# Optimization experiments

Hardware: AMD Instinct MI355X
Metric: run time of the kernel (lower is better)

Reference implementation:

```python
import jax, jax.numpy as jnp
import numpy as np

N_NODES = 50000
N_EDGES = 800000
IN, S1, S2, S3 = 64, 128, 64, 32


def _lin_init(key, fan_in, fan_out):
    kw, kb = jax.random.split(key)
    s = 1.0 / np.sqrt(fan_in)
    W = jax.random.uniform(kw, (fan_in, fan_out), minval=-s, maxval=s, dtype=jnp.float32)
    b = jax.random.uniform(kb, (fan_out,), minval=-s, maxval=s, dtype=jnp.float32)
    return W, b


def setup_inputs() -> dict:
    key = jax.random.key(0)
    ks = jax.random.split(key, 11)
    x = jax.random.normal(ks[0], (N_NODES, IN), dtype=jnp.float32)
    src = jax.random.randint(ks[1], (N_EDGES,), 0, N_NODES)
    dst = jax.random.randint(ks[2], (N_EDGES,), 0, N_NODES)
    W_n1, b_n1 = _lin_init(ks[3], IN, S1)
    W_c1, b_c1 = _lin_init(ks[4], S1, S2)
    W_n2, b_n2 = _lin_init(ks[5], S1, S2)
    W_c2, b_c2 = _lin_init(ks[6], S2, S3)
    W_n3, b_n3 = _lin_init(ks[7], S2, S3)
    W_c3, b_c3 = _lin_init(ks[8], S3, 1)
    W_g1, b_g1 = _lin_init(ks[9], S2, S3)
    W_g2, b_g2 = _lin_init(ks[10], S3, 1)
    return {
        'pre_node_embedding': x, 'src': src, 'dst': dst,
        'W_n1': W_n1, 'b_n1': b_n1, 'W_c1': W_c1, 'b_c1': b_c1,
        'W_n2': W_n2, 'b_n2': b_n2, 'W_c2': W_c2, 'b_c2': b_c2,
        'W_n3': W_n3, 'b_n3': b_n3, 'W_c3': W_c3, 'b_c3': b_c3,
        'W_g1': W_g1, 'b_g1': b_g1, 'W_g2': W_g2, 'b_g2': b_g2,
    }


def _node_update(W, b, emb, src, dst, n_nodes):
    # gather neighbor states along edges, scatter-add onto destinations
    agg = jax.ops.segment_sum(emb[src], dst, num_segments=n_nodes)  # [N, d_in]
    return jax.nn.sigmoid((emb + agg) @ W + b)                      # [N, d_out]


def _conduit_update(W, b, emb, src, dst):
    # conduit (edge) embedding from its two endpoint nodes
    return jax.nn.sigmoid((emb[src] + emb[dst]) @ W + b)            # [E, d_out]


def reference(pre_node_embedding, src, dst,
              W_n1, b_n1, W_c1, b_c1, W_n2, b_n2, W_c2, b_c2,
              W_n3, b_n3, W_c3, b_c3, W_g1, b_g1, W_g2, b_g2):
    n = pre_node_embedding.shape[0]
    h1 = _node_update(W_n1, b_n1, pre_node_embedding, src, dst, n)  # [N, S1]
    c1 = _conduit_update(W_c1, b_c1, h1, src, dst)                  # [E, S2]
    h2 = _node_update(W_n2, b_n2, h1, src, dst, n)                  # [N, S2]
    c2 = _conduit_update(W_c2, b_c2, h2, src, dst)                  # [E, S3]
    g1 = jax.nn.sigmoid(c1 @ W_g1 + b_g1 + c2)                      # [E, S3]
    h3 = _node_update(W_n3, b_n3, h2, src, dst, n)                  # [N, S3]
    c3 = _conduit_update(W_c3, b_c3, h3, src, dst)                  # [E, 1]
    out = jax.nn.sigmoid(g1 @ W_g2 + b_g2 + c3)                     # [E, 1]
    return out
```

## Files before the change

### kernel.cpp

```cpp
#include <hip/hip_runtime.h>

#define N_NODES 50000
#define N_EDGES 800000
#define CVT_B 6250
#define NODE_B ((N_NODES + 63) / 64)
#define EDGE_B (N_EDGES / 128)
#define NB 196
#define FILL_B 196
#define FILL_CHUNK 4096

typedef _Float16 h2 __attribute__((ext_vector_type(2)));
typedef _Float16 f16x8 __attribute__((ext_vector_type(8)));
typedef float f32x4 __attribute__((ext_vector_type(4)));

__device__ __forceinline__ float sigf(float v) {
  return __builtin_amdgcn_rcpf(1.0f + __expf(-v));
}
__device__ __forceinline__ unsigned packh2(float a, float b) {
  return __builtin_bit_cast(unsigned, __builtin_amdgcn_cvt_pkrtz(a, b));
}
__device__ __forceinline__ float2 unpackh2(unsigned u) {
  h2 p = __builtin_bit_cast(h2, u);
  return make_float2((float)p.x, (float)p.y);
}
__device__ __forceinline__ void acc8(float* a, uint4 v) {
  float2 p0 = unpackh2(v.x), p1 = unpackh2(v.y);
  float2 p2 = unpackh2(v.z), p3 = unpackh2(v.w);
  a[0] += p0.x; a[1] += p0.y; a[2] += p1.x; a[3] += p1.y;
  a[4] += p2.x; a[5] += p2.y; a[6] += p3.x; a[7] += p3.y;
}
__device__ __forceinline__ unsigned addpk(unsigned a, unsigned b) {
  h2 r = __builtin_bit_cast(h2, a) + __builtin_bit_cast(h2, b);
  return __builtin_bit_cast(unsigned, r);
}
#define MFMA16(A, B, C) __builtin_amdgcn_mfma_f32_16x16x32_f16(A, __builtin_bit_cast(f16x8, B), C, 0, 0, 0)

__global__ __launch_bounds__(256) void prep_kernel(
    const float* __restrict__ x, unsigned* __restrict__ x16,
    const float* __restrict__ Wn1, const float* __restrict__ Wn2,
    const float* __restrict__ Wc1, const float* __restrict__ Wn3,
    const float* __restrict__ Wc2, const float* __restrict__ Wg1,
    uint4* __restrict__ Wn1f, uint4* __restrict__ Wn2f, uint4* __restrict__ Wc1f,
    uint4* __restrict__ Wn3f, uint4* __restrict__ Wc2f, uint4* __restrict__ Wg1f)
{
  int b = blockIdx.x;
  if (b < CVT_B) {
    int i = b * 256 + threadIdx.x;
    float2 v = ((const float2*)x)[i];
    x16[i] = packh2(v.x, v.y);
  } else {
    int lane = threadIdx.x & 63, w = threadIdx.x >> 6;
    int n15 = lane & 15, chunk = lane >> 4;
    if (w == 0) {
#pragma unroll
      for (int f = 0; f < 16; ++f) {
        int nt = f >> 1, ks = f & 1;
        int n = nt * 16 + n15;
        f16x8 vv;
#pragma unroll
        for (int i = 0; i < 8; ++i) vv[i] = (_Float16)Wn1[(ks * 32 + chunk * 8 + i) * 128 + n];
        Wn1f[f * 64 + lane] = __builtin_bit_cast(uint4, vv);
      }
    } else if (w == 1) {
#pragma unroll
      for (int f = 0; f < 16; ++f) {
        int nt = f >> 2, ks = f & 3;
        int n = nt * 16 + n15;
        f16x8 vv;
#pragma unroll
        for (int i = 0; i < 8; ++i) vv[i] = (_Float16)Wn2[(ks * 32 + chunk * 8 + i) * 64 + n];
        Wn2f[f * 64 + lane] = __builtin_bit_cast(uint4, vv);
      }
    } else if (w == 2) {
#pragma unroll
      for (int f = 0; f < 16; ++f) {
        int nt = f >> 2, ks = f & 3;
        int n = nt * 16 + n15;
        f16x8 vv;
#pragma unroll
        for (int i = 0; i < 8; ++i) vv[i] = (_Float16)Wc1[(ks * 32 + chunk * 8 + i) * 64 + n];
        Wc1f[f * 64 + lane] = __builtin_bit_cast(uint4, vv);
      }
    } else {
#pragma unroll
      for (int f = 0; f < 4; ++f) {
        int nt = f >> 1, ks = f & 1;
        int n = nt * 16 + n15;
        f16x8 v3, vc;
#pragma unroll
        for (int i = 0; i < 8; ++i) {
          int k = ks * 32 + chunk * 8 + i;
          v3[i] = (_Float16)Wn3[k * 32 + n];
          vc[i] = (_Float16)Wc2[k * 32 + n];
        }
        Wn3f[f * 64 + lane] = __builtin_bit_cast(uint4, v3);
        Wc2f[f * 64 + lane] = __builtin_bit_cast(uint4, vc);
      }
#pragma unroll
      for (int ks = 0; ks < 2; ++ks)
#pragma unroll
        for (int nh = 0; nh < 2; ++nh) {
          f16x8 vv;
#pragma unroll
          for (int i = 0; i < 8; ++i)
            vv[i] = (_Float16)Wg1[(ks * 32 + chunk * 8 + i) * 32 + nh * 16 + n15];
          Wg1f[(ks * 2 + nh) * 64 + lane] = __builtin_bit_cast(uint4, vv);
        }
    }
  }
}

__global__ __launch_bounds__(256) void fill1_kernel(
    const int* __restrict__ dst, int* __restrict__ histM)
{
  __shared__ int hist[NB];
  int tid = threadIdx.x, bid = blockIdx.x;
  if (tid < NB) hist[tid] = 0;
  __syncthreads();
  int ebase = bid * FILL_CHUNK;
#pragma unroll
  for (int it = 0; it < FILL_CHUNK / 256; ++it) {
    int e = ebase + it * 256 + tid;
    if (e < N_EDGES) atomicAdd(&hist[dst[e] >> 8], 1);
  }
  __syncthreads();
  if (tid < NB) histM[bid * NB + tid] = hist[tid];
}

__global__ __launch_bounds__(256) void scanA_kernel(
    const int* __restrict__ histM, int* __restrict__ colOff,
    int* __restrict__ bucketBase)
{
  int j = threadIdx.x, lane = j & 63, w = j >> 6;
  int total = 0;
  if (j < NB)
    for (int i = 0; i < FILL_B; ++i) total += histM[i * NB + j];
  int x = total;
#pragma unroll
  for (int off = 1; off < 64; off <<= 1) {
    int y = __shfl_up(x, off);
    if (lane >= off) x += y;
  }
  __shared__ int ws[4];
  if (lane == 63) ws[w] = x;
  __syncthreads();
  int woff = 0;
#pragma unroll
  for (int k = 0; k < 4; ++k) if (k < w) woff += ws[k];
  int excl = woff + x - total;
  if (j < NB) {
    bucketBase[j] = excl;
    int running = excl;
    for (int i = 0; i < FILL_B; ++i) {
      colOff[i * NB + j] = running;
      running += histM[i * NB + j];
    }
    if (j == NB - 1) bucketBase[NB] = running;
  }
}

__global__ __launch_bounds__(256) void fill2_kernel(
    const int* __restrict__ src, const int* __restrict__ dst,
    const int* __restrict__ colOff, uint2* __restrict__ cem)
{
  __shared__ int cur[NB];
  int tid = threadIdx.x, bid = blockIdx.x;
  if (tid < NB) cur[tid] = colOff[bid * NB + tid];
  __syncthreads();
  int ebase = bid * FILL_CHUNK;
#pragma unroll
  for (int it = 0; it < FILL_CHUNK / 256; ++it) {
    int e = ebase + it * 256 + tid;
    if (e < N_EDGES) {
      int s = src[e], d = dst[e];
      int pos = atomicAdd(&cur[d >> 8], 1);
      cem[pos] = make_uint2((unsigned)s, ((unsigned)(d & 255) << 20) | (unsigned)e);
    }
  }
}

__global__ __launch_bounds__(256) void fill3_kernel(
    const uint2* __restrict__ cem, const int* __restrict__ bucketBase,
    uint2* __restrict__ ce, int* __restrict__ rowptr, int* __restrict__ did)
{
  __shared__ int cnt[256], curs[256], ws[4];
  int j = blockIdx.x, tid = threadIdx.x;
  int base = bucketBase[j], endb = bucketBase[j + 1];
  cnt[tid] = 0;
  __syncthreads();
  for (int k = base + tid; k < endb; k += 256)
    atomicAdd(&cnt[(cem[k].y >> 20) & 255], 1);
  __syncthreads();
  int v = cnt[tid];
  int lane = tid & 63, w = tid >> 6;
  int x = v;
#pragma unroll
  for (int off = 1; off < 64; off <<= 1) {
    int y = __shfl_up(x, off);
    if (lane >= off) x += y;
  }
  if (lane == 63) ws[w] = x;
  __syncthreads();
  int woff = 0;
#pragma unroll
  for (int k = 0; k < 4; ++k) if (k < w) woff += ws[k];
  int ex = woff + x - v;
  curs[tid] = ex;
  int n = j * 256 + tid;
  if (n < N_NODES) {
    rowptr[n + 1] = base + ex + v;
    if (n == 0) rowptr[0] = 0;
    for (int k2 = 0; k2 < v; ++k2) did[base + ex + k2] = n;
  }
  __syncthreads();
  for (int k = base + tid; k < endb; k += 256) {
    uint2 r = cem[k];
    int dlow = (r.y >> 20) & 255;
    int pos = base + atomicAdd(&curs[dlow], 1);
    ce[pos] = make_uint2(r.x, r.y & 0xFFFFFu);
  }
}

__global__ __launch_bounds__(256) void gather1_kernel(
    const unsigned* __restrict__ X16, const int* __restrict__ rowptr,
    const int* __restrict__ ce2, unsigned* __restrict__ T16)
{
  int w = threadIdx.x >> 6, lane = threadIdx.x & 63;
  int n = blockIdx.x * 4 + w;
  if (n >= N_NODES) return;
  int beg = rowptr[n], end = rowptr[n + 1];
  int q = lane >> 3, c = lane & 7;
  const uint4* feat4 = (const uint4*)X16;
  float a[8] = {0.f, 0.f, 0.f, 0.f, 0.f, 0.f, 0.f, 0.f};
  for (int k0 = beg; k0 < end; k0 += 64) {
    int kk = k0 + lane;
    int cv = (kk < end) ? ce2[2 * kk] : 0;
    int m = end - k0; if (m > 64) m = 64;
    int e = 0;
#pragma unroll 2
    for (; e + 7 < m; e += 8) {
      int se = __shfl(cv, e + q);
      acc8(a, feat4[(size_t)se * 8 + c]);
    }
    int r = m - e;
    if (r) {
      int idx = e + q; if (idx >= m) idx = m - 1;
      int se = __shfl(cv, idx);
      uint4 v = feat4[(size_t)se * 8 + c];
      if (q < r) acc8(a, v);
    }
  }
#pragma unroll
  for (int j = 0; j < 8; ++j) {
    a[j] += __shfl_xor(a[j], 32);
    a[j] += __shfl_xor(a[j], 16);
    a[j] += __shfl_xor(a[j], 8);
  }
  if (q == 0) {
    uint4 xv = ((const uint4*)X16)[(size_t)n * 8 + c];
    float2 x0 = unpackh2(xv.x), x1 = unpackh2(xv.y);
    float2 x2 = unpackh2(xv.z), x3 = unpackh2(xv.w);
    uint4 o;
    o.x = packh2(a[0] + x0.x, a[1] + x0.y);
    o.y = packh2(a[2] + x1.x, a[3] + x1.y);
    o.z = packh2(a[4] + x2.x, a[5] + x2.y);
    o.w = packh2(a[6] + x3.x, a[7] + x3.y);
    ((uint4*)T16)[(size_t)n * 8 + c] = o;
  }
}

__global__ __launch_bounds__(256) void gather2_kernel(
    const unsigned* __restrict__ Q2u, const int* __restrict__ rowptr,
    const int* __restrict__ ce2, const float* __restrict__ bn2,
    unsigned* __restrict__ H2)
{
  int w = threadIdx.x >> 6, lane = threadIdx.x & 63;
  int n = blockIdx.x * 4 + w;
  if (n >= N_NODES) return;
  int beg = rowptr[n], end = rowptr[n + 1];
  int q = lane >> 3, c = lane & 7;
  const uint4* feat4 = (const uint4*)Q2u;
  float a[8] = {0.f, 0.f, 0.f, 0.f, 0.f, 0.f, 0.f, 0.f};
  for (int k0 = beg; k0 < end; k0 += 64) {
    int kk = k0 + lane;
    int cv = (kk < end) ? ce2[2 * kk] : 0;
    int m = end - k0; if (m > 64) m = 64;
    int e = 0;
#pragma unroll 2
    for (; e + 7 < m; e += 8) {
      int se = __shfl(cv, e + q);
      acc8(a, feat4[(size_t)se * 8 + c]);
    }
    int r = m - e;
    if (r) {
      int idx = e + q; if (idx >= m) idx = m - 1;
      int se = __shfl(cv, idx);
      uint4 v = feat4[(size_t)se * 8 + c];
      if (q < r) acc8(a, v);
    }
  }
#pragma unroll
  for (int j = 0; j < 8; ++j) {
    a[j] += __shfl_xor(a[j], 32);
    a[j] += __shfl_xor(a[j], 16);
    a[j] += __shfl_xor(a[j], 8);
  }
  if (q == 0) {
    uint4 qv = ((const uint4*)Q2u)[(size_t)n * 8 + c];
    float4 bnA = ((const float4*)bn2)[2 * c];
    float4 bnB = ((const float4*)bn2)[2 * c + 1];
    float2 q0 = unpackh2(qv.x), q1 = unpackh2(qv.y);
    float2 q2 = unpackh2(qv.z), q3 = unpackh2(qv.w);
    uint4 o;
    o.x = packh2(sigf(a[0] + q0.x + bnA.x), sigf(a[1] + q0.y + bnA.y));
    o.y = packh2(sigf(a[2] + q1.x + bnA.z), sigf(a[3] + q1.y + bnA.w));
    o.z = packh2(sigf(a[4] + q2.x + bnB.x), sigf(a[5] + q2.y + bnB.y));
    o.w = packh2(sigf(a[6] + q3.x + bnB.z), sigf(a[7] + q3.y + bnB.w));
    ((uint4*)H2)[(size_t)n * 8 + c] = o;
  }
}

__global__ __launch_bounds__(256) void gather3_kernel(
    const unsigned* __restrict__ Q3u, const int* __restrict__ rowptr,
    const int* __restrict__ ce2, const float* __restrict__ bn3,
    const float* __restrict__ Wc3, _Float16* __restrict__ P3h)
{
  int w = threadIdx.x >> 6, lane = threadIdx.x & 63;
  int n = blockIdx.x * 4 + w;
  if (n >= N_NODES) return;
  int beg = rowptr[n], end = rowptr[n + 1];
  int q = lane >> 2, c = lane & 3;
  const uint4* feat4 = (const uint4*)Q3u;
  float a[8] = {0.f, 0.f, 0.f, 0.f, 0.f, 0.f, 0.f, 0.f};
  for (int k0 = beg; k0 < end; k0 += 64) {
    int kk = k0 + lane;
    int cv = (kk < end) ? ce2[2 * kk] : 0;
    int m = end - k0; if (m > 64) m = 64;
    int e = 0;
#pragma unroll 2
    for (; e + 15 < m; e += 16) {
      int se = __shfl(cv, e + q);
      acc8(a, feat4[(size_t)se * 4 + c]);
    }
    int r = m - e;
    if (r) {
      int idx = e + q; if (idx >= m) idx = m - 1;
      int se = __shfl(cv, idx);
      uint4 v = feat4[(size_t)se * 4 + c];
      if (q < r) acc8(a, v);
    }
  }
#pragma unroll
  for (int j = 0; j < 8; ++j) {
    a[j] += __shfl_xor(a[j], 32);
    a[j] += __shfl_xor(a[j], 16);
    a[j] += __shfl_xor(a[j], 8);
    a[j] += __shfl_xor(a[j], 4);
  }
  if (q == 0) {
    uint4 qv = feat4[(size_t)n * 4 + c];
    float4 bnA = ((const float4*)bn3)[2 * c], bnB = ((const float4*)bn3)[2 * c + 1];
    float4 wcA = ((const float4*)Wc3)[2 * c], wcB = ((const float4*)Wc3)[2 * c + 1];
    float2 q0 = unpackh2(qv.x), q1 = unpackh2(qv.y);
    float2 q2 = unpackh2(qv.z), q3 = unpackh2(qv.w);
    float p = sigf(a[0] + q0.x + bnA.x) * wcA.x + sigf(a[1] + q0.y + bnA.y) * wcA.y
            + sigf(a[2] + q1.x + bnA.z) * wcA.z + sigf(a[3] + q1.y + bnA.w) * wcA.w
            + sigf(a[4] + q2.x + bnB.x) * wcB.x + sigf(a[5] + q2.y + bnB.y) * wcB.y
            + sigf(a[6] + q3.x + bnB.z) * wcB.z + sigf(a[7] + q3.y + bnB.w) * wcB.w;
    p += __shfl_xor(p, 1); p += __shfl_xor(p, 2);
    if (c == 0) P3h[n] = (_Float16)p;
  }
}

__global__ __launch_bounds__(256) void node1_kernel(
    const unsigned* __restrict__ T16,
    const uint4* __restrict__ Wn1f, const uint4* __restrict__ Wn2f,
    const uint4* __restrict__ Wc1f, const float* __restrict__ bn1,
    _Float16* __restrict__ Q2h, _Float16* __restrict__ P1h)
{
  __shared__ __align__(16) _Float16 t_lds[64 * 72];
  __shared__ __align__(16) _Float16 h1_lds[64 * 136];
  int tid = threadIdx.x;
  int lane = tid & 63, w = tid >> 6;
  int nbase = blockIdx.x * 64;

#pragma unroll
  for (int rep = 0; rep < 2; ++rep) {
    int uidx = rep * 1024 + tid * 4;
    int node = uidx >> 5, c = uidx & 31;
    int gn = nbase + node; if (gn > N_NODES - 1) gn = N_NODES - 1;
    uint4 tv = *(const uint4*)(T16 + (size_t)gn * 32 + c);
    *(uint4*)(t_lds + node * 72 + c * 2) = tv;
  }
  __syncthreads();

  int row16 = lane & 15, chunk = lane >> 4;
  uint4 b1[2][2];
#pragma unroll
  for (int ntl = 0; ntl < 2; ++ntl)
#pragma unroll
    for (int ks = 0; ks < 2; ++ks)
      b1[ntl][ks] = Wn1f[((2 * w + ntl) * 2 + ks) * 64 + lane];

  f32x4 acc[4][2];
#pragma unroll
  for (int mt = 0; mt < 4; ++mt)
#pragma unroll
    for (int ntl = 0; ntl < 2; ++ntl) acc[mt][ntl] = (f32x4){0.f, 0.f, 0.f, 0.f};
#pragma unroll
  for (int mt = 0; mt < 4; ++mt) {
    const _Float16* ab = t_lds + (mt * 16 + row16) * 72 + chunk * 8;
    f16x8 A0 = *(const f16x8*)ab;
    f16x8 A1 = *(const f16x8*)(ab + 32);
#pragma unroll
    for (int ntl = 0; ntl < 2; ++ntl) {
      acc[mt][ntl] = MFMA16(A0, b1[ntl][0], acc[mt][ntl]);
      acc[mt][ntl] = MFMA16(A1, b1[ntl][1], acc[mt][ntl]);
    }
  }
  float bnv0 = bn1[w * 32 + row16], bnv1 = bn1[w * 32 + 16 + row16];
#pragma unroll
  for (int mt = 0; mt < 4; ++mt)
#pragma unroll
    for (int r = 0; r < 4; ++r) {
      int rowl = mt * 16 + chunk * 4 + r;
      h1_lds[rowl * 136 + w * 32 + row16]      = (_Float16)sigf(acc[mt][0][r] + bnv0);
      h1_lds[rowl * 136 + w * 32 + 16 + row16] = (_Float16)sigf(acc[mt][1][r] + bnv1);
    }
  __syncthreads();

#pragma unroll
  for (int job = 0; job < 2; ++job) {
    const uint4* Wf = job ? Wc1f : Wn2f;
    uint4 bf[4];
#pragma unroll
    for (int ks = 0; ks < 4; ++ks) bf[ks] = Wf[(w * 4 + ks) * 64 + lane];
    f32x4 a2[4];
#pragma unroll
    for (int mt = 0; mt < 4; ++mt) a2[mt] = (f32x4){0.f, 0.f, 0.f, 0.f};
#pragma unroll
    for (int mt = 0; mt < 4; ++mt) {
      const _Float16* hb = h1_lds + (mt * 16 + row16) * 136 + chunk * 8;
#pragma unroll
      for (int ks = 0; ks < 4; ++ks) {
        f16x8 A = *(const f16x8*)(hb + ks * 32);
        a2[mt] = MFMA16(A, bf[ks], a2[mt]);
      }
    }
    _Float16* op = job ? P1h : Q2h;
#pragma unroll
    for (int mt = 0; mt < 4; ++mt)
#pragma unroll
      for (int r = 0; r < 4; ++r) {
        int gn = nbase + mt * 16 + chunk * 4 + r;
        if (gn < N_NODES) op[(size_t)gn * 64 + w * 16 + row16] = (_Float16)a2[mt][r];
      }
  }
}

__global__ __launch_bounds__(256) void node2_kernel(
    const unsigned* __restrict__ H2,
    const uint4* __restrict__ Wn3f, const uint4* __restrict__ Wc2f,
    _Float16* __restrict__ Q3h, _Float16* __restrict__ P2h)
{
  __shared__ __align__(16) _Float16 t_lds[64 * 72];
  int tid = threadIdx.x, lane = tid & 63, w = tid >> 6;
  int nbase = blockIdx.x * 64;
#pragma unroll
  for (int rep = 0; rep < 2; ++rep) {
    int uidx = rep * 1024 + tid * 4;
    int node = uidx >> 5, c = uidx & 31;
    int gn = nbase + node; if (gn > N_NODES - 1) gn = N_NODES - 1;
    uint4 tv = *(const uint4*)(H2 + (size_t)gn * 32 + c);
    *(uint4*)(t_lds + node * 72 + c * 2) = tv;
  }
  __syncthreads();
  int row16 = lane & 15, chunk = lane >> 4;
  int mat = w >> 1, nt = w & 1;
  const uint4* Wf = mat ? Wc2f : Wn3f;
  uint4 bf0 = Wf[(nt * 2 + 0) * 64 + lane];
  uint4 bf1 = Wf[(nt * 2 + 1) * 64 + lane];
  f32x4 a2[4];
#pragma unroll
  for (int mt = 0; mt < 4; ++mt) a2[mt] = (f32x4){0.f, 0.f, 0.f, 0.f};
#pragma unroll
  for (int mt = 0; mt < 4; ++mt) {
    const _Float16* ab = t_lds + (mt * 16 + row16) * 72 + chunk * 8;
    f16x8 A0 = *(const f16x8*)ab;
    f16x8 A1 = *(const f16x8*)(ab + 32);
    a2[mt] = MFMA16(A0, bf0, a2[mt]);
    a2[mt] = MFMA16(A1, bf1, a2[mt]);
  }
  _Float16* op = mat ? P2h : Q3h;
#pragma unroll
  for (int mt = 0; mt < 4; ++mt)
#pragma unroll
    for (int r = 0; r < 4; ++r) {
      int gn = nbase + mt * 16 + chunk * 4 + r;
      if (gn < N_NODES) op[(size_t)gn * 32 + nt * 16 + row16] = (_Float16)a2[mt][r];
    }
}

__global__ __launch_bounds__(256) void edge_kernel(
    const uint2* __restrict__ ce, const int* __restrict__ did,
    const unsigned* __restrict__ P1_16, const unsigned* __restrict__ P2_16,
    const _Float16* __restrict__ P3_16, const uint4* __restrict__ Bfrag,
    const float* __restrict__ bc1, const float* __restrict__ bc2,
    const float* __restrict__ bc3, const float* __restrict__ bg1,
    const float* __restrict__ Wg2, const float* __restrict__ bg2,
    float* __restrict__ out)
{
  __shared__ __align__(16) _Float16 sbuf[4][32 * 104];
  __shared__ int eidx[4][64];
  __shared__ int eido[4][32];
  int lane = threadIdx.x & 63;
  int w = threadIdx.x >> 6;
  int b = blockIdx.x;
  int xcd = b & 7, idx = b >> 3;
  int swz = (xcd < 2 ? xcd * 782 : 2 * 782 + (xcd - 2) * 781) + idx;
  int ebase = swz * 128 + w * 32;
  _Float16* wb = &sbuf[w][0];

  int e32 = lane & 31;
  int myi;
  if (lane < 32) {
    uint2 cv2 = ce[ebase + e32];
    myi = (int)cv2.x;
    eido[w][e32] = (int)cv2.y;
  } else {
    myi = did[ebase + e32];
  }
  eidx[w][lane] = myi;

  f16x8 Bf[2][2];
#pragma unroll
  for (int ks = 0; ks < 2; ++ks)
#pragma unroll
    for (int nh = 0; nh < 2; ++nh)
      Bf[ks][nh] = __builtin_bit_cast(f16x8, Bfrag[(ks * 2 + nh) * 64 + lane]);

  {
    float p3v = (float)P3_16[myi];
    float pair = __shfl_xor(p3v, 32);
    if (lane < 32) wb[e32 * 104 + 96] = (_Float16)(p3v + pair);
  }
  {
    int c = lane & 7, q = lane >> 3;
    unsigned b10 = packh2(bc1[8 * c],     bc1[8 * c + 1]);
    unsigned b11 = packh2(bc1[8 * c + 2], bc1[8 * c + 3]);
    unsigned b12 = packh2(bc1[8 * c + 4], bc1[8 * c + 5]);
    unsigned b13 = packh2(bc1[8 * c + 6], bc1[8 * c + 7]);
#pragma unroll
    for (int it = 0; it < 4; ++it) {
      int e = 8 * it + q;
      int s = eidx[w][e];
      int d = eidx[w][32 + e];
      uint4 ps = *(const uint4*)(P1_16 + (size_t)s * 32 + 4 * c);
      uint4 pd = *(const uint4*)(P1_16 + (size_t)d * 32 + 4 * c);
      h2 v0 = __builtin_bit_cast(h2, addpk(addpk(ps.x, pd.x), b10));
      h2 v1 = __builtin_bit_cast(h2, addpk(addpk(ps.y, pd.y), b11));
      h2 v2 = __builtin_bit_cast(h2, addpk(addpk(ps.z, pd.z), b12));
      h2 v3 = __builtin_bit_cast(h2, addpk(addpk(ps.w, pd.w), b13));
      uint4 o;
      o.x = packh2(sigf((float)v0.x), sigf((float)v0.y));
      o.y = packh2(sigf((float)v1.x), sigf((float)v1.y));
      o.z = packh2(sigf((float)v2.x), sigf((float)v2.y));
      o.w = packh2(sigf((float)v3.x), sigf((float)v3.y));
      *(uint4*)(wb + e * 104 + 8 * c) = o;
    }
  }
  {
    int c = lane & 3, q = lane >> 2;
    unsigned b20 = packh2(bc2[8 * c],     bc2[8 * c + 1]);
    unsigned b21 = packh2(bc2[8 * c + 2], bc2[8 * c + 3]);
    unsigned b22 = packh2(bc2[8 * c + 4], bc2[8 * c + 5]);
    unsigned b23 = packh2(bc2[8 * c + 6], bc2[8 * c + 7]);
#pragma unroll
    for (int it = 0; it < 2; ++it) {
      int e = 16 * it + q;
      int s = eidx[w][e];
      int d = eidx[w][32 + e];
      uint4 ps = *(const uint4*)(P2_16 + (size_t)s * 16 + 4 * c);
      uint4 pd = *(const uint4*)(P2_16 + (size_t)d * 16 + 4 * c);
      h2 v0 = __builtin_bit_cast(h2, addpk(addpk(ps.x, pd.x), b20));
      h2 v1 = __builtin_bit_cast(h2, addpk(addpk(ps.y, pd.y), b21));
      h2 v2 = __builtin_bit_cast(h2, addpk(addpk(ps.z, pd.z), b22));
      h2 v3 = __builtin_bit_cast(h2, addpk(addpk(ps.w, pd.w), b23));
      uint4 o;
      o.x = packh2(sigf((float)v0.x), sigf((float)v0.y));
      o.y = packh2(sigf((float)v1.x), sigf((float)v1.y));
      o.z = packh2(sigf((float)v2.x), sigf((float)v2.y));
      o.w = packh2(sigf((float)v3.x), sigf((float)v3.y));
      *(uint4*)(wb + e * 104 + 64 + 8 * c) = o;
    }
  }

  int row = lane & 15, chunk = lane >> 4;
  float bg1v0 = bg1[row], bg1v1 = bg1[16 + row];
  float wg2v0 = Wg2[row], wg2v1 = Wg2[16 + row];
  float bg2v = bg2[0], bc3v = bc3[0];
#pragma unroll
  for (int g = 0; g < 2; ++g) {
    const _Float16* abase = wb + (16 * g + row) * 104 + chunk * 8;
    f16x8 A0 = *(const f16x8*)abase;
    f16x8 A1 = *(const f16x8*)(abase + 32);
    f32x4 acc0 = {0.f, 0.f, 0.f, 0.f}, acc1 = {0.f, 0.f, 0.f, 0.f};
    acc0 = __builtin_amdgcn_mfma_f32_16x16x32_f16(A0, Bf[0][0], acc0, 0, 0, 0);
    acc1 = __builtin_amdgcn_mfma_f32_16x16x32_f16(A0, Bf[0][1], acc1, 0, 0, 0);
    acc0 = __builtin_amdgcn_mfma_f32_16x16x32_f16(A1, Bf[1][0], acc0, 0, 0, 0);
    acc1 = __builtin_amdgcn_mfma_f32_16x16x32_f16(A1, Bf[1][1], acc1, 0, 0, 0);
#pragma unroll
    for (int r = 0; r < 4; ++r) {
      int e = 16 * g + chunk * 4 + r;
      float c2a = (float)wb[e * 104 + 64 + row];
      float c2b = (float)wb[e * 104 + 80 + row];
      float v0 = sigf(acc0[r] + bg1v0 + c2a) * wg2v0;
      float v1 = sigf(acc1[r] + bg1v1 + c2b) * wg2v1;
      float part = v0 + v1;
      part += __shfl_xor(part, 1);
      part += __shfl_xor(part, 2);
      part += __shfl_xor(part, 4);
      part += __shfl_xor(part, 8);
      float c3v = (float)wb[e * 104 + 96];
      if (row == 0)
        out[eido[w][e]] = sigf(part + bg2v + sigf(c3v + bc3v));
    }
  }
}

extern "C" void kernel_launch(void* const* d_in, const int* in_sizes, int n_in,
                              void* d_out, int out_size, void* d_ws, size_t ws_size,
                              hipStream_t stream)
{
  const float* x   = (const float*)d_in[0];
  const int*   src = (const int*)d_in[1];
  const int*   dst = (const int*)d_in[2];
  const float* Wn1 = (const float*)d_in[3];
  const float* bn1 = (const float*)d_in[4];
  const float* Wc1 = (const float*)d_in[5];
  const float* bc1 = (const float*)d_in[6];
  const float* Wn2 = (const float*)d_in[7];
  const float* bn2 = (const float*)d_in[8];
  const float* Wc2 = (const float*)d_in[9];
  const float* bc2 = (const float*)d_in[10];
  const float* Wn3 = (const float*)d_in[11];
  const float* bn3 = (const float*)d_in[12];
  const float* Wc3 = (const float*)d_in[13];
  const float* bc3 = (const float*)d_in[14];
  const float* Wg1 = (const float*)d_in[15];
  const float* bg1 = (const float*)d_in[16];
  const float* Wg2 = (const float*)d_in[17];
  const float* bg2 = (const float*)d_in[18];
  float* out = (float*)d_out;

  char* base = (char*)d_ws;
  unsigned* TMP16 = (unsigned*)base; base += (size_t)N_NODES * 32 * 4;
  unsigned* X16   = (unsigned*)base; base += (size_t)N_NODES * 32 * 4;
  unsigned* Q2_16 = (unsigned*)base; base += (size_t)N_NODES * 32 * 4;
  unsigned* P1_16 = (unsigned*)base; base += (size_t)N_NODES * 32 * 4;
  unsigned* Q3_16 = (unsigned*)base; base += (size_t)N_NODES * 16 * 4;
  unsigned* P2_16 = (unsigned*)base; base += (size_t)N_NODES * 16 * 4;
  _Float16* P3_16 = (_Float16*)base; base += ((size_t)N_NODES * 2 + 15) / 16 * 16;
  int* rowptr = (int*)base;          base += (size_t)(N_NODES + 1) * 4 + 12;
  uint2* ce   = (uint2*)base;        base += (size_t)N_EDGES * 8;
  uint2* cem  = (uint2*)base;        base += (size_t)N_EDGES * 8;
  int* did    = (int*)base;          base += (size_t)N_EDGES * 4;
  int* histM  = (int*)base;          base += (size_t)FILL_B * NB * 4;
  int* colOff = (int*)base;          base += (size_t)FILL_B * NB * 4;
  int* bucketBase = (int*)base;      base += (size_t)(NB + 1) * 4 + 12;
  uint4* Wg1f = (uint4*)base;        base += 4 * 64 * 16;
  uint4* Wn1f = (uint4*)base;        base += 16 * 64 * 16;
  uint4* Wn2f = (uint4*)base;        base += 16 * 64 * 16;
  uint4* Wc1f = (uint4*)base;        base += 16 * 64 * 16;
  uint4* Wn3f = (uint4*)base;        base += 4 * 64 * 16;
  uint4* Wc2f = (uint4*)base;        base += 4 * 64 * 16;

  prep_kernel<<<CVT_B + 1, 256, 0, stream>>>(x, X16,
      Wn1, Wn2, Wc1, Wn3, Wc2, Wg1, Wn1f, Wn2f, Wc1f, Wn3f, Wc2f, Wg1f);
  fill1_kernel<<<FILL_B, 256, 0, stream>>>(dst, histM);
  scanA_kernel<<<1, 256, 0, stream>>>(histM, colOff, bucketBase);
  fill2_kernel<<<FILL_B, 256, 0, stream>>>(src, dst, colOff, cem);
  fill3_kernel<<<NB, 256, 0, stream>>>(cem, bucketBase, ce, rowptr, did);

  gather1_kernel<<<(N_NODES + 3) / 4, 256, 0, stream>>>(X16, rowptr, (const int*)ce, TMP16);
  node1_kernel<<<NODE_B, 256, 0, stream>>>(TMP16, Wn1f, Wn2f, Wc1f, bn1,
      (_Float16*)Q2_16, (_Float16*)P1_16);
  gather2_kernel<<<(N_NODES + 3) / 4, 256, 0, stream>>>(Q2_16, rowptr, (const int*)ce, bn2, TMP16);
  node2_kernel<<<NODE_B, 256, 0, stream>>>(TMP16, Wn3f, Wc2f,
      (_Float16*)Q3_16, (_Float16*)P2_16);
  gather3_kernel<<<(N_NODES + 3) / 4, 256, 0, stream>>>(Q3_16, rowptr, (const int*)ce, bn3, Wc3, P3_16);
  edge_kernel<<<EDGE_B, 256, 0, stream>>>(ce, did, P1_16, P2_16, P3_16, Wg1f,
      bc1, bc2, bc3, bg1, Wg2, bg2, out);
}
```

Measured before the change: 178.9 us.

## Compact edge indices to 16-bit, pack dst into ce, fold histogram into prep

Source and destination node ids (both under 65536) are packed into one 32-bit word of the CSR edge record, which removes the separate per-edge dst array and the per-node loop that wrote it. A separate 16-bit column array is added so the three gather kernels read 2 bytes per neighbor instead of a strided 4-byte field out of 8-byte records. The dst histogram pass is merged into the prep kernel as extra blocks, saving one launch. The packing depends on node counts fitting in 16 bits.

```diff
diff --git a/kernel.cpp b/kernel.cpp
--- a/kernel.cpp
+++ b/kernel.cpp
@@ -37,6 +37,7 @@
 
 __global__ __launch_bounds__(256) void prep_kernel(
     const float* __restrict__ x, unsigned* __restrict__ x16,
+    const int* __restrict__ dst, int* __restrict__ histM,
     const float* __restrict__ Wn1, const float* __restrict__ Wn2,
     const float* __restrict__ Wc1, const float* __restrict__ Wn3,
     const float* __restrict__ Wc2, const float* __restrict__ Wg1,
@@ -48,6 +49,19 @@
     int i = b * 256 + threadIdx.x;
     float2 v = ((const float2*)x)[i];
     x16[i] = packh2(v.x, v.y);
+  } else if (b < CVT_B + FILL_B) {
+    __shared__ int hist[NB];
+    int tid = threadIdx.x, bid = b - CVT_B;
+    if (tid < NB) hist[tid] = 0;
+    __syncthreads();
+    int ebase = bid * FILL_CHUNK;
+#pragma unroll
+    for (int it = 0; it < FILL_CHUNK / 256; ++it) {
+      int e = ebase + it * 256 + tid;
+      if (e < N_EDGES) atomicAdd(&hist[dst[e] >> 8], 1);
+    }
+    __syncthreads();
+    if (tid < NB) histM[bid * NB + tid] = hist[tid];
   } else {
     int lane = threadIdx.x & 63, w = threadIdx.x >> 6;
     int n15 = lane & 15, chunk = lane >> 4;
@@ -110,23 +124,6 @@
   }
 }
 
-__global__ __launch_bounds__(256) void fill1_kernel(
-    const int* __restrict__ dst, int* __restrict__ histM)
-{
-  __shared__ int hist[NB];
-  int tid = threadIdx.x, bid = blockIdx.x;
-  if (tid < NB) hist[tid] = 0;
-  __syncthreads();
-  int ebase = bid * FILL_CHUNK;
-#pragma unroll
-  for (int it = 0; it < FILL_CHUNK / 256; ++it) {
-    int e = ebase + it * 256 + tid;
-    if (e < N_EDGES) atomicAdd(&hist[dst[e] >> 8], 1);
-  }
-  __syncthreads();
-  if (tid < NB) histM[bid * NB + tid] = hist[tid];
-}
-
 __global__ __launch_bounds__(256) void scanA_kernel(
     const int* __restrict__ histM, int* __restrict__ colOff,
     int* __restrict__ bucketBase)
@@ -181,7 +178,8 @@
 
 __global__ __launch_bounds__(256) void fill3_kernel(
     const uint2* __restrict__ cem, const int* __restrict__ bucketBase,
-    uint2* __restrict__ ce, int* __restrict__ rowptr, int* __restrict__ did)
+    uint2* __restrict__ ce, unsigned short* __restrict__ col16,
+    int* __restrict__ rowptr)
 {
   __shared__ int cnt[256], curs[256], ws[4];
   int j = blockIdx.x, tid = threadIdx.x;
@@ -210,20 +208,21 @@
   if (n < N_NODES) {
     rowptr[n + 1] = base + ex + v;
     if (n == 0) rowptr[0] = 0;
-    for (int k2 = 0; k2 < v; ++k2) did[base + ex + k2] = n;
   }
   __syncthreads();
   for (int k = base + tid; k < endb; k += 256) {
     uint2 r = cem[k];
     int dlow = (r.y >> 20) & 255;
     int pos = base + atomicAdd(&curs[dlow], 1);
-    ce[pos] = make_uint2(r.x, r.y & 0xFFFFFu);
+    unsigned d = (unsigned)(j * 256 + dlow);
+    ce[pos] = make_uint2(r.x | (d << 16), r.y & 0xFFFFFu);
+    col16[pos] = (unsigned short)r.x;
   }
 }
 
 __global__ __launch_bounds__(256) void gather1_kernel(
     const unsigned* __restrict__ X16, const int* __restrict__ rowptr,
-    const int* __restrict__ ce2, unsigned* __restrict__ T16)
+    const unsigned short* __restrict__ col16, unsigned* __restrict__ T16)
 {
   int w = threadIdx.x >> 6, lane = threadIdx.x & 63;
   int n = blockIdx.x * 4 + w;
@@ -234,7 +233,7 @@
   float a[8] = {0.f, 0.f, 0.f, 0.f, 0.f, 0.f, 0.f, 0.f};
   for (int k0 = beg; k0 < end; k0 += 64) {
     int kk = k0 + lane;
-    int cv = (kk < end) ? ce2[2 * kk] : 0;
+    int cv = (kk < end) ? (int)col16[kk] : 0;
     int m = end - k0; if (m > 64) m = 64;
     int e = 0;
 #pragma unroll 2
@@ -271,7 +270,7 @@
 
 __global__ __launch_bounds__(256) void gather2_kernel(
     const unsigned* __restrict__ Q2u, const int* __restrict__ rowptr,
-    const int* __restrict__ ce2, const float* __restrict__ bn2,
+    const unsigned short* __restrict__ col16, const float* __restrict__ bn2,
     unsigned* __restrict__ H2)
 {
   int w = threadIdx.x >> 6, lane = threadIdx.x & 63;
@@ -283,7 +282,7 @@
   float a[8] = {0.f, 0.f, 0.f, 0.f, 0.f, 0.f, 0.f, 0.f};
   for (int k0 = beg; k0 < end; k0 += 64) {
     int kk = k0 + lane;
-    int cv = (kk < end) ? ce2[2 * kk] : 0;
+    int cv = (kk < end) ? (int)col16[kk] : 0;
     int m = end - k0; if (m > 64) m = 64;
     int e = 0;
 #pragma unroll 2
@@ -322,7 +321,7 @@
 
 __global__ __launch_bounds__(256) void gather3_kernel(
     const unsigned* __restrict__ Q3u, const int* __restrict__ rowptr,
-    const int* __restrict__ ce2, const float* __restrict__ bn3,
+    const unsigned short* __restrict__ col16, const float* __restrict__ bn3,
     const float* __restrict__ Wc3, _Float16* __restrict__ P3h)
 {
   int w = threadIdx.x >> 6, lane = threadIdx.x & 63;
@@ -334,7 +333,7 @@
   float a[8] = {0.f, 0.f, 0.f, 0.f, 0.f, 0.f, 0.f, 0.f};
   for (int k0 = beg; k0 < end; k0 += 64) {
     int kk = k0 + lane;
-    int cv = (kk < end) ? ce2[2 * kk] : 0;
+    int cv = (kk < end) ? (int)col16[kk] : 0;
     int m = end - k0; if (m > 64) m = 64;
     int e = 0;
 #pragma unroll 2
@@ -502,7 +501,7 @@
 }
 
 __global__ __launch_bounds__(256) void edge_kernel(
-    const uint2* __restrict__ ce, const int* __restrict__ did,
+    const uint2* __restrict__ ce,
     const unsigned* __restrict__ P1_16, const unsigned* __restrict__ P2_16,
     const _Float16* __restrict__ P3_16, const uint4* __restrict__ Bfrag,
     const float* __restrict__ bc1, const float* __restrict__ bc2,
@@ -522,15 +521,12 @@
   _Float16* wb = &sbuf[w][0];
 
   int e32 = lane & 31;
-  int myi;
-  if (lane < 32) {
-    uint2 cv2 = ce[ebase + e32];
-    myi = (int)cv2.x;
-    eido[w][e32] = (int)cv2.y;
-  } else {
-    myi = did[ebase + e32];
-  }
+  uint2 cv2 = ce[ebase + e32];
+  int sv = (int)(cv2.x & 0xFFFFu);
+  int dv = (int)(cv2.x >> 16);
+  int myi = (lane < 32) ? sv : dv;
   eidx[w][lane] = myi;
+  if (lane < 32) eido[w][e32] = (int)cv2.y;
 
   f16x8 Bf[2][2];
 #pragma unroll
@@ -664,7 +660,7 @@
   int* rowptr = (int*)base;          base += (size_t)(N_NODES + 1) * 4 + 12;
   uint2* ce   = (uint2*)base;        base += (size_t)N_EDGES * 8;
   uint2* cem  = (uint2*)base;        base += (size_t)N_EDGES * 8;
-  int* did    = (int*)base;          base += (size_t)N_EDGES * 4;
+  unsigned short* col16 = (unsigned short*)base; base += ((size_t)N_EDGES * 2 + 15) / 16 * 16;
   int* histM  = (int*)base;          base += (size_t)FILL_B * NB * 4;
   int* colOff = (int*)base;          base += (size_t)FILL_B * NB * 4;
   int* bucketBase = (int*)base;      base += (size_t)(NB + 1) * 4 + 12;
@@ -675,20 +671,19 @@
   uint4* Wn3f = (uint4*)base;        base += 4 * 64 * 16;
   uint4* Wc2f = (uint4*)base;        base += 4 * 64 * 16;
 
-  prep_kernel<<<CVT_B + 1, 256, 0, stream>>>(x, X16,
+  prep_kernel<<<CVT_B + FILL_B + 1, 256, 0, stream>>>(x, X16, dst, histM,
       Wn1, Wn2, Wc1, Wn3, Wc2, Wg1, Wn1f, Wn2f, Wc1f, Wn3f, Wc2f, Wg1f);
-  fill1_kernel<<<FILL_B, 256, 0, stream>>>(dst, histM);
   scanA_kernel<<<1, 256, 0, stream>>>(histM, colOff, bucketBase);
   fill2_kernel<<<FILL_B, 256, 0, stream>>>(src, dst, colOff, cem);
-  fill3_kernel<<<NB, 256, 0, stream>>>(cem, bucketBase, ce, rowptr, did);
-
-  gather1_kernel<<<(N_NODES + 3) / 4, 256, 0, stream>>>(X16, rowptr, (const int*)ce, TMP16);
+  fill3_kernel<<<NB, 256, 0, stream>>>(cem, bucketBase, ce, col16, rowptr);
+
+  gather1_kernel<<<(N_NODES + 3) / 4, 256, 0, stream>>>(X16, rowptr, col16, TMP16);
   node1_kernel<<<NODE_B, 256, 0, stream>>>(TMP16, Wn1f, Wn2f, Wc1f, bn1,
       (_Float16*)Q2_16, (_Float16*)P1_16);
-  gather2_kernel<<<(N_NODES + 3) / 4, 256, 0, stream>>>(Q2_16, rowptr, (const int*)ce, bn2, TMP16);
+  gather2_kernel<<<(N_NODES + 3) / 4, 256, 0, stream>>>(Q2_16, rowptr, col16, bn2, TMP16);
   node2_kernel<<<NODE_B, 256, 0, stream>>>(TMP16, Wn3f, Wc2f,
       (_Float16*)Q3_16, (_Float16*)P2_16);
-  gather3_kernel<<<(N_NODES + 3) / 4, 256, 0, stream>>>(Q3_16, rowptr, (const int*)ce, bn3, Wc3, P3_16);
-  edge_kernel<<<EDGE_B, 256, 0, stream>>>(ce, did, P1_16, P2_16, P3_16, Wg1f,
+  gather3_kernel<<<(N_NODES + 3) / 4, 256, 0, stream>>>(Q3_16, rowptr, col16, bn3, Wc3, P3_16);
+  edge_kernel<<<EDGE_B, 256, 0, stream>>>(ce, P1_16, P2_16, P3_16, Wg1f,
       bc1, bc2, bc3, bg1, Wg2, bg2, out);
 }
```

Result: no change. 178.0 us (-0.5%).
